# Performance work log

Hardware: AMD Instinct MI355X
Metric: run time of the kernel (lower is better)

## Reference

```python
import jax, jax.numpy as jnp
import numpy as np

TOP_K = 48
NUM_RBF = 16
MAX_REL = 32  # max_relative_feature


def _rbf(D):
    # D: [...], expand into NUM_RBF Gaussian basis functions over [2, 22] Angstrom
    mu = jnp.linspace(2.0, 22.0, NUM_RBF)
    sigma = (22.0 - 2.0) / NUM_RBF
    return jnp.exp(-(((D[..., None] - mu) / sigma) ** 2))


def _gather_nodes(C, E_idx):
    # C: [B,L,3], E_idx: [B,L,K] -> [B,L,K,3]
    return jax.vmap(lambda c, idx: c[idx])(C, E_idx)


def _pair_rbf(A, Bc, E_idx):
    # RBF of ||A_i - Bc_j|| for j in neighbors(i); identical math to torch's
    # full [B,L,L] cdist followed by gather_edges, but gathers coords first.
    Bg = _gather_nodes(Bc, E_idx)
    D = jnp.sqrt(jnp.sum((A[:, :, None, :] - Bg) ** 2, -1) + 1e-6)
    return _rbf(D)


def setup_inputs() -> dict:
    key = jax.random.key(0)
    ks = jax.random.split(key, 8)
    B, L = 4, 1024
    X = jax.random.normal(ks[0], (B, L, 4, 3), jnp.float32)
    mask = jnp.ones((B, L), jnp.float32)
    residue_idx = jnp.arange(B * L, dtype=jnp.int32).reshape(B, L)
    chain_labels = jax.random.randint(ks[1], (B, L), 0, 4, dtype=jnp.int32)
    W_pos = jax.random.normal(ks[2], (16, 2 * MAX_REL + 2), jnp.float32) * 0.1
    b_pos = jnp.zeros((16,), jnp.float32)
    W_edge = jax.random.normal(ks[3], (128, 16 + 25 * NUM_RBF), jnp.float32) * 0.05
    ln_g = jnp.ones((128,), jnp.float32)
    ln_b = jnp.zeros((128,), jnp.float32)
    return dict(X=X, mask=mask, residue_idx=residue_idx, chain_labels=chain_labels,
                W_pos=W_pos, b_pos=b_pos, W_edge=W_edge, ln_g=ln_g, ln_b=ln_b)


def reference(X, mask, residue_idx, chain_labels, W_pos, b_pos, W_edge, ln_g, ln_b):
    # backbone atoms
    N = X[:, :, 0]; Ca = X[:, :, 1]; C = X[:, :, 2]; O = X[:, :, 3]
    b = Ca - N
    c = C - Ca
    a = jnp.cross(b, c)
    Cb = -0.58273431 * a + 0.56802827 * b - 0.54067466 * c + Ca

    # _dist: masked Ca-Ca pairwise distances, k nearest neighbors
    mask2 = mask[:, None, :] * mask[:, :, None]          # [B,L,L]
    dX = Ca[:, None, :, :] - Ca[:, :, None, :]
    D = mask2 * jnp.sqrt(jnp.sum(dX ** 2, -1) + 1e-6)
    D_max = jnp.max(D, -1, keepdims=True)
    D_adjust = D + (1.0 - mask2) * D_max
    K = min(TOP_K, X.shape[1])
    negD, E_idx = jax.lax.top_k(-D_adjust, K)            # smallest-K distances
    D_neighbors = -negD                                  # [B,L,K]

    # 25 atom-pair RBF blocks (order matches torch source)
    pairs = [(N, N), (C, C), (O, O), (Cb, Cb), (Ca, N), (Ca, C), (Ca, O), (Ca, Cb),
             (N, C), (N, O), (N, Cb), (Cb, C), (Cb, O), (O, C), (N, Ca), (C, Ca),
             (O, Ca), (Cb, Ca), (C, N), (O, N), (Cb, N), (C, Cb), (O, Cb), (C, O)]
    RBFs = [_rbf(D_neighbors)] + [_pair_rbf(A, Bc, E_idx) for A, Bc in pairs]
    RBFs = jnp.concatenate(RBFs, -1)                     # [B,L,K,25*NUM_RBF]

    # positional encodings
    offset = residue_idx[:, :, None] - residue_idx[:, None, :]
    offset = jnp.take_along_axis(offset, E_idx, axis=2)  # [B,L,K]
    d_chains = (chain_labels[:, :, None] == chain_labels[:, None, :]).astype(jnp.int32)
    E_chains = jnp.take_along_axis(d_chains, E_idx, axis=2)
    d = jnp.clip(offset + MAX_REL, 0, 2 * MAX_REL)
    d = d * E_chains + (1 - E_chains) * (2 * MAX_REL + 1)
    # one_hot(d, 66) @ W_pos.T + b_pos == row gather of W_pos.T
    E_pos = W_pos.T[d] + b_pos                           # [B,L,K,16]

    E = jnp.concatenate([E_pos, RBFs], -1)               # [B,L,K,416]
    E = jnp.einsum('blkf,ef->blke', E, W_edge)           # edge_embedding (no bias)
    mu = jnp.mean(E, -1, keepdims=True)
    var = jnp.var(E, -1, keepdims=True)
    E = (E - mu) / jnp.sqrt(var + 1e-5) * ln_g + ln_b    # LayerNorm
    return E, E_idx
```

## Files before the change

kernel.cpp:

```cpp
#include <hip/hip_runtime.h>
#include <stdint.h>

#define LSEQ 1024
#define NB 4
#define KNB 48
#define NFEAT 416
#define NOUT 128
#define NNODE (NB*LSEQ)

typedef float f32x4 __attribute__((ext_vector_type(4)));
typedef short s16x8 __attribute__((ext_vector_type(8)));

__device__ float4 g_atoms[NNODE*5];
__device__ ushort g_wbf[NOUT*NFEAT];
__device__ ushort g_wpt[66*16];
__device__ int    g_nbr[NNODE*KNB];
__device__ float  g_dnb[NNODE*KNB];

__constant__ int cPA[24] = {0,2,3,4,1,1,1,1,0,0,0,4,4,3,0,2,3,4,2,3,4,2,3,2};
__constant__ int cPB[24] = {0,2,3,4,0,2,3,4,2,3,4,2,3,2,1,1,1,1,0,0,0,4,4,3};
__constant__ float cC[16] = {
  0.0f, 1.28119724f, 2.56239447f, 3.84359171f,
  5.12478894f, 6.40598618f, 7.68718342f, 8.96838065f,
  10.24957789f, 11.53077512f, 12.81197236f, 14.09316960f,
  15.37436683f, 16.65556407f, 17.93676131f, 19.21795854f};

__device__ __forceinline__ ushort f2bf(float x) {
  unsigned u = __float_as_uint(x);
  u += 0x7fffu + ((u >> 16) & 1u);
  return (ushort)(u >> 16);
}
__device__ __forceinline__ unsigned pack2bf(float lo, float hi) {
  return __builtin_amdgcn_perm(__float_as_uint(hi), __float_as_uint(lo), 0x07060302u);
}

#define DPP_ADD_F(x, CTRL) { int _y = __builtin_amdgcn_mov_dpp(__float_as_int(x), CTRL, 0xF, 0xF, true); x += __int_as_float(_y); }
#define DPP_MIN_U(x, CTRL) { unsigned _y = (unsigned)__builtin_amdgcn_mov_dpp((int)(x), CTRL, 0xF, 0xF, true); x = min(x, _y); }

__device__ __forceinline__ unsigned wave_umin(unsigned x) {
  DPP_MIN_U(x, 0x128) DPP_MIN_U(x, 0x124) DPP_MIN_U(x, 0x122) DPP_MIN_U(x, 0x121)
  x = min(x, (unsigned)__shfl_xor((int)x, 16, 64));
  x = min(x, (unsigned)__shfl_xor((int)x, 32, 64));
  return x;
}

__global__ __launch_bounds__(256) void k_front(
    const float* __restrict__ X, const float* __restrict__ mask,
    const float* __restrict__ W, const float* __restrict__ Wpos,
    const float* __restrict__ bpos, float* __restrict__ outIdx)
{
  __shared__ float4 sca[LSEQ];
  __shared__ unsigned qhi[4][64][17];
  __shared__ unsigned qlo[4][64][17];
  int blk = blockIdx.x, tid = threadIdx.x;

  if (blk >= 1024) {
    int pb = blk - 1024;
    if (pb < 16) {
      int t = pb*256 + tid;
      const float* p = X + (size_t)t*12;
      float nx=p[0],ny=p[1],nz=p[2];
      float cax=p[3],cay=p[4],caz=p[5];
      float cx=p[6],cy=p[7],cz=p[8];
      float ox=p[9],oy=p[10],oz=p[11];
      float bx=cax-nx, by=cay-ny, bz=caz-nz;
      float ex=cx-cax, ey=cy-cay, ez=cz-caz;
      float ax2 = by*ez - bz*ey;
      float ay2 = bz*ex - bx*ez;
      float az2 = bx*ey - by*ex;
      float cbx = -0.58273431f*ax2 + 0.56802827f*bx - 0.54067466f*ex + cax;
      float cby = -0.58273431f*ay2 + 0.56802827f*by - 0.54067466f*ey + cay;
      float cbz = -0.58273431f*az2 + 0.56802827f*bz - 0.54067466f*ez + caz;
      g_atoms[t*5+0] = make_float4(nx,ny,nz,0.f);
      g_atoms[t*5+1] = make_float4(cax,cay,caz,0.f);
      g_atoms[t*5+2] = make_float4(cx,cy,cz,0.f);
      g_atoms[t*5+3] = make_float4(ox,oy,oz,0.f);
      g_atoms[t*5+4] = make_float4(cbx,cby,cbz,0.f);
    } else if (pb < 32) {
      int base = (pb-16)*3328 + tid;
      #pragma unroll
      for (int q = 0; q < 13; ++q) g_wbf[base + q*256] = f2bf(W[base + q*256]);
    } else {
      for (int t = tid; t < 66*16; t += 256) {
        int d = t >> 4, c = t & 15;
        g_wpt[t] = f2bf(Wpos[c*66 + d] + bpos[c]);
      }
    }
    return;
  }

  int b = blk >> 8, chunk = blk & 255;
  for (int t = tid; t < LSEQ; t += 256) {
    const float* p = X + (size_t)(b*LSEQ + t)*12 + 3;
    sca[t] = make_float4(p[0], p[1], p[2], mask[b*LSEQ + t]);
  }
  __syncthreads();
  int wv = tid >> 6, lane = tid & 63;
  int i = chunk*4 + wv;
  float4 ci = sca[i];
  float  mi = ci.w;

  float Dv[16]; float dmax = 0.f;
  #pragma unroll
  for (int q = 0; q < 16; ++q) {
    int j = lane + (q << 6);
    float4 cj = sca[j];
    float dx = __fsub_rn(cj.x, ci.x);
    float dy = __fsub_rn(cj.y, ci.y);
    float dz = __fsub_rn(cj.z, ci.z);
    float s  = __fadd_rn(__fadd_rn(__fmul_rn(dx,dx), __fmul_rn(dy,dy)), __fmul_rn(dz,dz));
    float sq = __fsqrt_rn(__fadd_rn(s, 1e-6f));
    float d  = __fmul_rn(__fmul_rn(mi, cj.w), sq);
    Dv[q] = d;
    dmax = fmaxf(dmax, d);
  }
  #pragma unroll
  for (int o = 32; o; o >>= 1) dmax = fmaxf(dmax, __shfl_xor(dmax, o, 64));

  unsigned long long key[16];
  #pragma unroll
  for (int q = 0; q < 16; ++q) {
    int j = lane + (q << 6);
    float m2   = __fmul_rn(mi, sca[j].w);
    float dadj = __fadd_rn(Dv[q], __fmul_rn(__fsub_rn(1.0f, m2), dmax));
    key[q] = ((unsigned long long)__float_as_uint(dadj) << 32) | (unsigned)j;
  }

  #pragma unroll
  for (int p = 1; p < 16; p <<= 1)
    #pragma unroll
    for (int k = p; k >= 1; k >>= 1)
      #pragma unroll
      for (int j = k & (p - 1); j + k < 16; j += 2*k)
        #pragma unroll
        for (int u = 0; u < k; ++u)
          if (u + j + k < 16 && ((u + j) / (2*p) == (u + j + k) / (2*p))) {
            unsigned long long a = key[u+j], c2 = key[u+j+k];
            if (a > c2) { key[u+j] = c2; key[u+j+k] = a; }
          }

  #pragma unroll
  for (int q = 0; q < 16; ++q) {
    qhi[wv][lane][q] = (unsigned)(key[q] >> 32);
    qlo[wv][lane][q] = (unsigned)key[q];
  }

  unsigned hhi = (unsigned)(key[0] >> 32), hlo = (unsigned)key[0];
  int pos = 0;
  size_t row = (size_t)(b*LSEQ + i);
  for (int k = 0; k < KNB; ++k) {
    unsigned mh = wave_umin(hhi);
    unsigned long long bmask = __ballot(hhi == mh);
    bool own;
    if (__popcll(bmask) == 1) {
      own = (hhi == mh);
    } else {
      unsigned jv = (hhi == mh) ? hlo : 0xFFFFFFFFu;
      unsigned mj = wave_umin(jv);
      own = (hhi == mh) && (hlo == mj);
    }
    if (own) {
      g_nbr[row*KNB + k] = (int)hlo;
      g_dnb[row*KNB + k] = __uint_as_float(mh);
      outIdx[row*KNB + k] = (float)(int)hlo;
      ++pos;
      if (pos < 16) { hhi = qhi[wv][lane][pos]; hlo = qlo[wv][lane][pos]; }
      else          { hhi = 0xFFFFFFFFu; hlo = 0xFFFFFFFFu; }
    }
  }
}

__global__ __launch_bounds__(256, 4) void k_edge(
    const int* __restrict__ ridx, const int* __restrict__ chain,
    const float* __restrict__ lng, const float* __restrict__ lnb,
    float* __restrict__ out)
{
  __shared__ __align__(16) ushort featb[KNB*256];
  __shared__ float4 atN[KNB*5];
  __shared__ float4 atI[5];
  __shared__ float  sdn[KNB];
  __shared__ int    sdd[KNB];
  __shared__ float2 sstat[KNB][4];
  __shared__ float2 rstat[KNB];

  int node = blockIdx.x;
  int b = node >> 10;
  size_t ebase = (size_t)node * KNB;
  int t = threadIdx.x;

  if (t < KNB) {
    int j = g_nbr[ebase + t];
    sdn[t] = g_dnb[ebase + t];
    int off = ridx[node] - ridx[b*LSEQ + j];
    bool same = (chain[node] == chain[b*LSEQ + j]);
    int dcl = min(max(off + 32, 0), 64);
    sdd[t] = same ? dcl : 65;
  }
  if (t >= 64 && t < 69) atI[t-64] = g_atoms[node*5 + (t-64)];
  for (int u = t; u < KNB*5; u += 256) {
    int k = u / 5, a = u % 5;
    atN[u] = g_atoms[(b*LSEQ + g_nbr[ebase + k])*5 + a];
  }
  __syncthreads();

  auto rbf_store = [&](int k, int slot, float d) {
    float u0 = __fmaf_rn(d, 0.96089793f, -1.92179585f);
    float e[16];
    #pragma unroll
    for (int m = 0; m < 16; ++m) {
      float u = u0 - cC[m];
      e[m] = __builtin_amdgcn_exp2f(-(u*u));
    }
    union { s16x8 v; unsigned w[4]; } a0, a1;
    #pragma unroll
    for (int q = 0; q < 4; ++q) {
      a0.w[q] = pack2bf(e[2*q],   e[2*q+1]);
      a1.w[q] = pack2bf(e[8+2*q], e[8+2*q+1]);
    }
    ushort* fp = &featb[k*256 + ((slot ^ (k & 7)) << 4)];
    *(s16x8*)fp       = a0.v;
    *(s16x8*)(fp + 8) = a1.v;
  };

  if (t < 96) {
    int k = t >> 1, h = t & 1;
    *(s16x8*)&featb[k*256 + ((0 ^ (k & 7)) << 4) + h*8] =
        *(const s16x8*)&g_wpt[sdd[k]*16 + h*8];
  }
  for (int u = t; u < KNB*13; u += 256) {
    int k = u / 13, p = u % 13;
    float d;
    if (p == 0) d = sdn[k];
    else {
      float4 A = atI[cPA[p-1]];
      float4 Bv = atN[k*5 + cPB[p-1]];
      float dx = A.x-Bv.x, dy = A.y-Bv.y, dz = A.z-Bv.z;
      d = sqrtf(dx*dx + dy*dy + dz*dz + 1e-6f);
    }
    rbf_store(k, p + 1, d);
  }
  __syncthreads();

  int ln = t & 63, wv = t >> 6;
  int fr = ln & 15, fq = ln >> 4;
  int n0 = wv * 32;
  f32x4 acc[3][2];
  #pragma unroll
  for (int mt = 0; mt < 3; ++mt) { acc[mt][0] = (f32x4)0.f; acc[mt][1] = (f32x4)0.f; }
  const ushort* w0 = &g_wbf[(n0 + fr)*NFEAT];
  const ushort* w1 = &g_wbf[(n0 + 16 + fr)*NFEAT];

#define GEMM_PASS(WOFF, NSTEPS)                                                     \
  {                                                                                 \
    s16x8 cw0 = *(const s16x8*)&w0[(WOFF) + fq*8];                                  \
    s16x8 cw1 = *(const s16x8*)&w1[(WOFF) + fq*8];                                  \
    _Pragma("unroll")                                                               \
    for (int s = 0; s < (NSTEPS); ++s) {                                            \
      int kk = s*32 + fq*8;                                                         \
      s16x8 nw0, nw1;                                                               \
      if (s + 1 < (NSTEPS)) {                                                       \
        nw0 = *(const s16x8*)&w0[(WOFF) + kk + 32];                                 \
        nw1 = *(const s16x8*)&w1[(WOFF) + kk + 32];                                 \
      }                                                                             \
      _Pragma("unroll")                                                             \
      for (int mt = 0; mt < 3; ++mt) {                                              \
        int row = mt*16 + fr;                                                       \
        s16x8 af = *(const s16x8*)&featb[row*256 + (((kk >> 4) ^ (fr & 7)) << 4) + (kk & 8)]; \
        acc[mt][0] = __builtin_amdgcn_mfma_f32_16x16x32_bf16(af, cw0, acc[mt][0], 0, 0, 0);   \
        acc[mt][1] = __builtin_amdgcn_mfma_f32_16x16x32_bf16(af, cw1, acc[mt][1], 0, 0, 0);   \
      }                                                                             \
      if (s + 1 < (NSTEPS)) { cw0 = nw0; cw1 = nw1; }                               \
    }                                                                               \
  }

  GEMM_PASS(0, 7)
  __syncthreads();

  for (int u = t; u < KNB*12; u += 256) {
    int k = u / 12, p = 13 + u % 12;
    float4 A = atI[cPA[p-1]];
    float4 Bv = atN[k*5 + cPB[p-1]];
    float dx = A.x-Bv.x, dy = A.y-Bv.y, dz = A.z-Bv.z;
    rbf_store(k, p - 13, sqrtf(dx*dx + dy*dy + dz*dz + 1e-6f));
  }
  __syncthreads();

  GEMM_PASS(224, 6)

  #pragma unroll
  for (int mt = 0; mt < 3; ++mt)
    #pragma unroll
    for (int i2 = 0; i2 < 4; ++i2) {
      float v0 = acc[mt][0][i2], v1 = acc[mt][1][i2];
      float s = v0 + v1, sq = v0*v0 + v1*v1;
      DPP_ADD_F(s, 0x128) DPP_ADD_F(s, 0x124) DPP_ADD_F(s, 0x122) DPP_ADD_F(s, 0x121)
      DPP_ADD_F(sq, 0x128) DPP_ADD_F(sq, 0x124) DPP_ADD_F(sq, 0x122) DPP_ADD_F(sq, 0x121)
      if (fr == 0) sstat[mt*16 + fq*4 + i2][wv] = make_float2(s, sq);
    }
  __syncthreads();
  if (t < KNB) {
    float s = 0.f, sq = 0.f;
    #pragma unroll
    for (int w = 0; w < 4; ++w) { float2 pp = sstat[t][w]; s += pp.x; sq += pp.y; }
    float mu  = s * (1.0f/128.0f);
    float var = sq * (1.0f/128.0f) - mu*mu;
    rstat[t] = make_float2(mu, rsqrtf(var + 1e-5f));
  }
  __syncthreads();
  float gn0 = lng[n0+fr], gn1 = lng[n0+16+fr];
  float bn0 = lnb[n0+fr], bn1 = lnb[n0+16+fr];
  #pragma unroll
  for (int mt = 0; mt < 3; ++mt)
    #pragma unroll
    for (int i2 = 0; i2 < 4; ++i2) {
      int row = mt*16 + fq*4 + i2;
      float2 mr = rstat[row];
      size_t ob = (ebase + row) * NOUT;
      out[ob + n0 + fr]      = (acc[mt][0][i2] - mr.x) * mr.y * gn0 + bn0;
      out[ob + n0 + 16 + fr] = (acc[mt][1][i2] - mr.x) * mr.y * gn1 + bn1;
    }
}

extern "C" void kernel_launch(void* const* d_in, const int* in_sizes, int n_in,
                              void* d_out, int out_size, void* d_ws, size_t ws_size,
                              hipStream_t stream) {
  const float* X     = (const float*)d_in[0];
  const float* mask  = (const float*)d_in[1];
  const int*   ridx  = (const int*)d_in[2];
  const int*   chain = (const int*)d_in[3];
  const float* Wpos  = (const float*)d_in[4];
  const float* bpos  = (const float*)d_in[5];
  const float* Wedge = (const float*)d_in[6];
  const float* lng   = (const float*)d_in[7];
  const float* lnb   = (const float*)d_in[8];
  float* out = (float*)d_out;
  float* outIdx = out + (size_t)NNODE*KNB*NOUT;

  k_front<<<dim3(1024 + 33), dim3(256), 0, stream>>>(X, mask, Wedge, Wpos, bpos, outIdx);
  k_edge<<<dim3(NNODE), dim3(256), 0, stream>>>(ridx, chain, lng, lnb, out);
}
```

Before: 82.97 us.

## Stage full feature tile in LDS and preload all weights into registers

The two-pass feature build and GEMM, which reused a half-size LDS buffer, becomes a single pass that writes all 26 feature slots into a 448-element-pitch LDS tile followed by one 13-step MFMA loop. All 13 weight fragments per thread are loaded into registers at kernel start, so global weight loads overlap with the neighbour gathers instead of sitting inside the GEMM loop. This removes two barriers and the reload pipeline, but it roughly doubles the LDS tile, raises register pressure, and lowers the launch-bounds occupancy target from 4 to 3. The XOR swizzle is narrowed from k&7 to k&3 to fit the new pitch.

```diff
diff --git a/kernel.cpp b/kernel.cpp
--- a/kernel.cpp
+++ b/kernel.cpp
@@ -7,6 +7,7 @@
 #define NFEAT 416
 #define NOUT 128
 #define NNODE (NB*LSEQ)
+#define FPITCH 448
 
 typedef float f32x4 __attribute__((ext_vector_type(4)));
 typedef short s16x8 __attribute__((ext_vector_type(8)));
@@ -170,12 +171,12 @@
   }
 }
 
-__global__ __launch_bounds__(256, 4) void k_edge(
+__global__ __launch_bounds__(256, 3) void k_edge(
     const int* __restrict__ ridx, const int* __restrict__ chain,
     const float* __restrict__ lng, const float* __restrict__ lnb,
     float* __restrict__ out)
 {
-  __shared__ __align__(16) ushort featb[KNB*256];
+  __shared__ __align__(16) ushort featb[KNB*FPITCH];
   __shared__ float4 atN[KNB*5];
   __shared__ float4 atI[5];
   __shared__ float  sdn[KNB];
@@ -187,6 +188,18 @@
   int b = node >> 10;
   size_t ebase = (size_t)node * KNB;
   int t = threadIdx.x;
+  int ln = t & 63, wv = t >> 6;
+  int fr = ln & 15, fq = ln >> 4;
+  int n0 = wv * 32;
+
+  const ushort* w0 = &g_wbf[(n0 + fr)*NFEAT + fq*8];
+  const ushort* w1 = &g_wbf[(n0 + 16 + fr)*NFEAT + fq*8];
+  s16x8 wr0[13], wr1[13];
+  #pragma unroll
+  for (int s = 0; s < 13; ++s) {
+    wr0[s] = *(const s16x8*)&w0[s*32];
+    wr1[s] = *(const s16x8*)&w1[s*32];
+  }
 
   if (t < KNB) {
     int j = g_nbr[ebase + t];
@@ -203,32 +216,13 @@
   }
   __syncthreads();
 
-  auto rbf_store = [&](int k, int slot, float d) {
-    float u0 = __fmaf_rn(d, 0.96089793f, -1.92179585f);
-    float e[16];
-    #pragma unroll
-    for (int m = 0; m < 16; ++m) {
-      float u = u0 - cC[m];
-      e[m] = __builtin_amdgcn_exp2f(-(u*u));
-    }
-    union { s16x8 v; unsigned w[4]; } a0, a1;
-    #pragma unroll
-    for (int q = 0; q < 4; ++q) {
-      a0.w[q] = pack2bf(e[2*q],   e[2*q+1]);
-      a1.w[q] = pack2bf(e[8+2*q], e[8+2*q+1]);
-    }
-    ushort* fp = &featb[k*256 + ((slot ^ (k & 7)) << 4)];
-    *(s16x8*)fp       = a0.v;
-    *(s16x8*)(fp + 8) = a1.v;
-  };
-
   if (t < 96) {
     int k = t >> 1, h = t & 1;
-    *(s16x8*)&featb[k*256 + ((0 ^ (k & 7)) << 4) + h*8] =
+    *(s16x8*)&featb[k*FPITCH + ((0 ^ (k & 3)) << 4) + h*8] =
         *(const s16x8*)&g_wpt[sdd[k]*16 + h*8];
   }
-  for (int u = t; u < KNB*13; u += 256) {
-    int k = u / 13, p = u % 13;
+  for (int u = t; u < KNB*25; u += 256) {
+    int k = u / 25, p = u % 25;
     float d;
     if (p == 0) d = sdn[k];
     else {
@@ -237,55 +231,39 @@
       float dx = A.x-Bv.x, dy = A.y-Bv.y, dz = A.z-Bv.z;
       d = sqrtf(dx*dx + dy*dy + dz*dz + 1e-6f);
     }
-    rbf_store(k, p + 1, d);
-  }
-  __syncthreads();
-
-  int ln = t & 63, wv = t >> 6;
-  int fr = ln & 15, fq = ln >> 4;
-  int n0 = wv * 32;
+    float u0 = __fmaf_rn(d, 0.96089793f, -1.92179585f);
+    float e[16];
+    #pragma unroll
+    for (int m = 0; m < 16; ++m) {
+      float uu = u0 - cC[m];
+      e[m] = __builtin_amdgcn_exp2f(-(uu*uu));
+    }
+    union { s16x8 v; unsigned w[4]; } a0, a1;
+    #pragma unroll
+    for (int q = 0; q < 4; ++q) {
+      a0.w[q] = pack2bf(e[2*q],   e[2*q+1]);
+      a1.w[q] = pack2bf(e[8+2*q], e[8+2*q+1]);
+    }
+    ushort* fp = &featb[k*FPITCH + (((p+1) ^ (k & 3)) << 4)];
+    *(s16x8*)fp       = a0.v;
+    *(s16x8*)(fp + 8) = a1.v;
+  }
+  __syncthreads();
+
   f32x4 acc[3][2];
   #pragma unroll
   for (int mt = 0; mt < 3; ++mt) { acc[mt][0] = (f32x4)0.f; acc[mt][1] = (f32x4)0.f; }
-  const ushort* w0 = &g_wbf[(n0 + fr)*NFEAT];
-  const ushort* w1 = &g_wbf[(n0 + 16 + fr)*NFEAT];
-
-#define GEMM_PASS(WOFF, NSTEPS)                                                     \
-  {                                                                                 \
-    s16x8 cw0 = *(const s16x8*)&w0[(WOFF) + fq*8];                                  \
-    s16x8 cw1 = *(const s16x8*)&w1[(WOFF) + fq*8];                                  \
-    _Pragma("unroll")                                                               \
-    for (int s = 0; s < (NSTEPS); ++s) {                                            \
-      int kk = s*32 + fq*8;                                                         \
-      s16x8 nw0, nw1;                                                               \
-      if (s + 1 < (NSTEPS)) {                                                       \
-        nw0 = *(const s16x8*)&w0[(WOFF) + kk + 32];                                 \
-        nw1 = *(const s16x8*)&w1[(WOFF) + kk + 32];                                 \
-      }                                                                             \
-      _Pragma("unroll")                                                             \
-      for (int mt = 0; mt < 3; ++mt) {                                              \
-        int row = mt*16 + fr;                                                       \
-        s16x8 af = *(const s16x8*)&featb[row*256 + (((kk >> 4) ^ (fr & 7)) << 4) + (kk & 8)]; \
-        acc[mt][0] = __builtin_amdgcn_mfma_f32_16x16x32_bf16(af, cw0, acc[mt][0], 0, 0, 0);   \
-        acc[mt][1] = __builtin_amdgcn_mfma_f32_16x16x32_bf16(af, cw1, acc[mt][1], 0, 0, 0);   \
-      }                                                                             \
-      if (s + 1 < (NSTEPS)) { cw0 = nw0; cw1 = nw1; }                               \
-    }                                                                               \
-  }
-
-  GEMM_PASS(0, 7)
-  __syncthreads();
-
-  for (int u = t; u < KNB*12; u += 256) {
-    int k = u / 12, p = 13 + u % 12;
-    float4 A = atI[cPA[p-1]];
-    float4 Bv = atN[k*5 + cPB[p-1]];
-    float dx = A.x-Bv.x, dy = A.y-Bv.y, dz = A.z-Bv.z;
-    rbf_store(k, p - 13, sqrtf(dx*dx + dy*dy + dz*dz + 1e-6f));
-  }
-  __syncthreads();
-
-  GEMM_PASS(224, 6)
+  #pragma unroll
+  for (int s = 0; s < 13; ++s) {
+    int kk = s*32 + fq*8;
+    #pragma unroll
+    for (int mt = 0; mt < 3; ++mt) {
+      int row = mt*16 + fr;
+      s16x8 af = *(const s16x8*)&featb[row*FPITCH + (((kk >> 4) ^ (fr & 3)) << 4) + (kk & 8)];
+      acc[mt][0] = __builtin_amdgcn_mfma_f32_16x16x32_bf16(af, wr0[s], acc[mt][0], 0, 0, 0);
+      acc[mt][1] = __builtin_amdgcn_mfma_f32_16x16x32_bf16(af, wr1[s], acc[mt][1], 0, 0, 0);
+    }
+  }
 
   #pragma unroll
   for (int mt = 0; mt < 3; ++mt)
```

New measurement: 98.03 us. +18.2%, slower.
